# Optimization experiments

Hardware: AMD Instinct MI355X
Metric: run time of the kernel (lower is better)

Reference implementation:

```python
import jax, jax.numpy as jnp
import numpy as np

N_NODES, NUM_GRAPHS, MAX_N = 65536, 512, 192
D, H = 512, 8
DH = D // H


def setup_inputs() -> dict:
    key = jax.random.key(0)
    ks = jax.random.split(key, 13)
    s = 1.0 / np.sqrt(D).astype(np.float32)
    return {
        "node_features": jax.random.normal(ks[0], (N_NODES, D), jnp.float32),
        "batch_indices": jnp.sort(jax.random.randint(ks[1], (N_NODES,), 0, NUM_GRAPHS)),
        "global_query": jax.random.normal(ks[2], (1, H, 1, DH), jnp.float32) * s,
        "w_q": jax.random.normal(ks[3], (D, D), jnp.float32) * s,
        "b_q": jax.random.normal(ks[4], (D,), jnp.float32) * 0.02,
        "w_k": jax.random.normal(ks[5], (D, D), jnp.float32) * s,
        "b_k": jax.random.normal(ks[6], (D,), jnp.float32) * 0.02,
        "w_v": jax.random.normal(ks[7], (D, D), jnp.float32) * s,
        "b_v": jax.random.normal(ks[8], (D,), jnp.float32) * 0.02,
        "w_o": jax.random.normal(ks[9], (D, D), jnp.float32) * s,
        "b_o": jax.random.normal(ks[10], (D,), jnp.float32) * 0.02,
        "w_p": jax.random.normal(ks[11], (D, D), jnp.float32) * s,
        "b_p": jax.random.normal(ks[12], (D,), jnp.float32) * 0.02,
    }


def reference(node_features, batch_indices, global_query, w_q, b_q, w_k, b_k,
              w_v, b_v, w_o, b_o, w_p, b_p):
    # ragged bookkeeping (batch_indices is sorted)
    counts = jax.ops.segment_sum(jnp.ones_like(batch_indices), batch_indices,
                                 num_segments=NUM_GRAPHS)            # [G]
    offsets = jnp.cumsum(counts) - counts                            # [G]
    pos = jnp.arange(N_NODES) - offsets[batch_indices]               # local node pos

    # pad nodes to dense [G, MAX_N, D]
    dense = jnp.zeros((NUM_GRAPHS, MAX_N, D), node_features.dtype)
    dense = dense.at[batch_indices, pos].set(node_features)
    mask = jnp.zeros((NUM_GRAPHS, MAX_N), bool).at[batch_indices, pos].set(True)

    # Faithful replication of torch's expand+reshape of global_query:
    # Q_in[g, t, d] = gq_flat[h*DH + d%DH] with h = (t*D + d) // (n_g*DH)
    gqf = global_query.reshape(H * DH)
    t = jnp.arange(MAX_N)[:, None]                                   # [MAX_N,1]
    d = jnp.arange(D)[None, :]                                       # [1,D]
    n = jnp.maximum(counts, 1)[:, None, None]                        # [G,1,1]
    h = jnp.clip((t * D + d)[None] // (n * DH), 0, H - 1)            # [G,MAX_N,D]
    q_in = gqf[h * DH + (d % DH)[None]]                              # [G,MAX_N,D]

    Q = (q_in @ w_q.T + b_q).reshape(NUM_GRAPHS, MAX_N, H, DH)
    K = (dense @ w_k.T + b_k).reshape(NUM_GRAPHS, MAX_N, H, DH)
    V = (dense @ w_v.T + b_v).reshape(NUM_GRAPHS, MAX_N, H, DH)

    scale = 1.0 / np.sqrt(DH).astype(np.float32)
    scores = jnp.einsum('gthd,gshd->ghts', Q, K) * scale             # [G,H,T,S]
    scores = jnp.where(mask[:, None, None, :], scores, -1e9)
    attn_w = jax.nn.softmax(scores, axis=-1)
    attn = jnp.einsum('ghts,gshd->gthd', attn_w, V).reshape(NUM_GRAPHS, MAX_N, D)
    attn = attn @ w_o.T + b_o

    denom = jnp.maximum(counts, 1).astype(attn.dtype)[:, None]
    pooled = (attn * mask[..., None].astype(attn.dtype)).sum(axis=1) / denom
    return jax.nn.relu(pooled @ w_p.T + b_p)                         # [G, D]
```

## Files before the change

### kernel.cpp

```cpp
#include <hip/hip_runtime.h>
#include <hip/hip_bf16.h>
#include <cstdint>

typedef __bf16 bf16;
typedef __attribute__((ext_vector_type(8))) __bf16 bf16x8;
typedef __attribute__((ext_vector_type(4))) __bf16 bf16x4;
typedef __attribute__((ext_vector_type(2))) __bf16 bf16x2;
typedef __attribute__((ext_vector_type(4))) float f32x4;

#define N_NODES    65536
#define NUM_GRAPHS 512
#define MAX_N      192
#define D          512
#define H          8
#define DH         64
#define UMAX       64
#define USTRIDE    132

__device__ __forceinline__ void gload_lds16(const void* g, void* l) {
    __builtin_amdgcn_global_load_lds((const __attribute__((address_space(1))) void*)g,
                                     (__attribute__((address_space(3))) void*)l, 16, 0, 0);
}

__global__ __launch_bounds__(256) void lb_kernel(const int* __restrict__ batch,
                                                 int* __restrict__ lb) {
    int g = blockIdx.x * 256 + threadIdx.x;
    if (g > NUM_GRAPHS) return;
    int lo = 0, hi = N_NODES;
    while (lo < hi) {
        int mid = (lo + hi) >> 1;
        if (batch[mid] < g) lo = mid + 1; else hi = mid;
    }
    lb[g] = lo;
}

__global__ __launch_bounds__(192) void dedup_kernel(const int* __restrict__ lb,
                                                    int* __restrict__ udata) {
    const int g = blockIdx.x;
    const int off = lb[g];
    const int n = min(lb[g + 1] - off, MAX_N);
    __shared__ int keys[MAX_N];
    __shared__ int ukey[UMAX], ucnt[UMAX];
    __shared__ int nu_s;
    const int t = threadIdx.x;
    if (t < n) {
        unsigned un = (unsigned)n;
        int key = 0;
        #pragma unroll
        for (int p = 0; p < 8; p++) key |= (int)(((unsigned)(8 * t + p)) / un) << (3 * p);
        keys[t] = key;
    }
    __syncthreads();
    if (t == 0) {
        int nu = 0;
        for (int s = 0; s < n; s++) {
            if (s == 0 || keys[s] != keys[s - 1]) {
                if (nu < UMAX) { ukey[nu] = keys[s]; ucnt[nu] = 0; nu++; }
            }
            ucnt[nu - 1] += 1;
        }
        nu_s = nu;
    }
    __syncthreads();
    const int nu = nu_s;
    int* base = udata + (size_t)g * USTRIDE;
    if (t == 0) base[0] = nu;
    if (t < nu) { base[1 + t] = ukey[t]; base[65 + t] = ucnt[t]; }
}

__global__ __launch_bounds__(256) void cvt_kernel(const float* __restrict__ src,
                                                  bf16* __restrict__ dst, int n) {
    int i = (blockIdx.x * 256 + threadIdx.x) * 4;
    if (i >= n) return;
    float4 v = *(const float4*)(src + i);
    bf16x4 o = {(bf16)v.x, (bf16)v.y, (bf16)v.z, (bf16)v.w};
    *(bf16x4*)(dst + i) = o;
}

__global__ __launch_bounds__(256) void p2_kernel(const float* __restrict__ gq,
                                                 const float* __restrict__ wq,
                                                 float* __restrict__ P2) {
    int h = blockIdx.x, p = blockIdx.y;
    __shared__ float gs[64];
    if (threadIdx.x < 64) gs[threadIdx.x] = gq[h * 64 + threadIdx.x];
    __syncthreads();
    for (int o = threadIdx.x; o < D; o += 256) {
        const float* wr = wq + (size_t)o * D + p * 64;
        float acc = 0.f;
        #pragma unroll 16
        for (int j = 0; j < 64; j++) acc += gs[j] * wr[j];
        P2[(size_t)(h * 8 + p) * D + o] = acc;
    }
}

__global__ __launch_bounds__(256) void wov_kernel(const float* __restrict__ wo,
                                                  const float* __restrict__ wv,
                                                  bf16* __restrict__ Wov) {
    const int ot = blockIdx.x;
    const int h  = blockIdx.y;
    __shared__ float wos[32 * 64];
    for (int idx = threadIdx.x; idx < 32 * 64; idx += 256) {
        int ol = idx >> 6, j = idx & 63;
        wos[idx] = wo[(size_t)(ot * 32 + ol) * D + h * 64 + j];
    }
    __syncthreads();
    const int c = threadIdx.x * 2;
    float acc0[32] = {}, acc1[32] = {};
    for (int j = 0; j < 64; j++) {
        float2 v2 = *(const float2*)(wv + (size_t)(h * 64 + j) * D + c);
        #pragma unroll
        for (int o = 0; o < 32; o++) {
            float wj = wos[o * 64 + j];
            acc0[o] += wj * v2.x; acc1[o] += wj * v2.y;
        }
    }
    #pragma unroll
    for (int o = 0; o < 32; o++) {
        bf16x2 r = {(bf16)acc0[o], (bf16)acc1[o]};
        *(bf16x2*)(Wov + (size_t)(ot * 32 + o) * 4096 + h * 512 + c) = r;
    }
}

__global__ __launch_bounds__(256) void cst_kernel(const float* __restrict__ wo,
                                                  const float* __restrict__ bv,
                                                  const float* __restrict__ bo,
                                                  float* __restrict__ cst) {
    int o = blockIdx.x * 256 + threadIdx.x;
    if (o >= D) return;
    const float* wr = wo + (size_t)o * D;
    float acc = bo[o];
    for (int d0 = 0; d0 < D; d0 += 4) {
        float4 wv4 = *(const float4*)(wr + d0);
        float4 b4  = *(const float4*)(bv + d0);
        acc += wv4.x * b4.x + wv4.y * b4.y + wv4.z * b4.z + wv4.w * b4.w;
    }
    cst[o] = acc;
}

__global__ __launch_bounds__(256) void k_gemm(const bf16* __restrict__ Ab,
                                              const bf16* __restrict__ Wkb,
                                              const float* __restrict__ bkb,
                                              bf16* __restrict__ Kout) {
    const int lin = blockIdx.x;
    const int xcd = lin & 7;
    const int idx = lin >> 3;
    const int nt  = idx & 3;
    const int ml  = idx >> 2;
    const int i0 = (xcd * 64 + ml) * 128;
    const int o0 = nt * 128;

    __shared__ char smem[16896];
    bf16* As = (bf16*)smem;
    bf16* Bs = (bf16*)(smem + 8192);
    const int tid = threadIdx.x;
    const int lane = tid & 63;
    const int w = tid >> 6;
    const int wm = w & 1, wn = w >> 1;
    const int fr = lane & 15, quad = lane >> 4;
    const bf16* gA = Ab + (size_t)(i0 + w * 32 + (lane >> 2)) * D + (lane & 3) * 8;
    const bf16* gB = Wkb + (size_t)(o0 + w * 32 + (lane >> 2)) * D + (lane & 3) * 8;
    bf16* lA = As + (w * 32) * 32;
    bf16* lB = Bs + (w * 32) * 32;

    f32x4 acc[4][4] = {};

    for (int kt = 0; kt < D; kt += 32) {
        __syncthreads();
        gload_lds16(gA + kt, lA);
        gload_lds16(gA + (size_t)16 * D + kt, lA + 16 * 32);
        gload_lds16(gB + kt, lB);
        gload_lds16(gB + (size_t)16 * D + kt, lB + 16 * 32);
        __syncthreads();
        bf16x8 fa[4], fb[4];
        #pragma unroll
        for (int mf = 0; mf < 4; mf++)
            fa[mf] = *(const bf16x8*)(As + (wm * 64 + mf * 16 + fr) * 32 + quad * 8);
        #pragma unroll
        for (int nf = 0; nf < 4; nf++)
            fb[nf] = *(const bf16x8*)(Bs + (wn * 64 + nf * 16 + fr) * 32 + quad * 8);
        #pragma unroll
        for (int mf = 0; mf < 4; mf++)
            #pragma unroll
            for (int nf = 0; nf < 4; nf++)
                acc[mf][nf] = __builtin_amdgcn_mfma_f32_16x16x32_bf16(fa[mf], fb[nf], acc[mf][nf], 0, 0, 0);
    }

    bf16* Cs = (bf16*)smem;
    #pragma unroll
    for (int pass = 0; pass < 2; pass++) {
        __syncthreads();
        if (wm == pass) {
            #pragma unroll
            for (int nf = 0; nf < 4; nf++) {
                const int col = wn * 64 + nf * 16 + fr;
                const float bs = bkb[o0 + col];
                #pragma unroll
                for (int mf = 0; mf < 4; mf++) {
                    #pragma unroll
                    for (int r = 0; r < 4; r++)
                        Cs[(mf * 16 + quad * 4 + r) * 132 + col] = (bf16)(acc[mf][nf][r] + bs);
                }
            }
        }
        __syncthreads();
        #pragma unroll
        for (int k = 0; k < 4; k++) {
            int idx2 = k * 256 + tid;
            int row = idx2 >> 4;
            int coff = (idx2 & 15) * 8;
            bf16x8 v = *(const bf16x8*)(Cs + row * 132 + coff);
            *(bf16x8*)(Kout + (size_t)(i0 + pass * 64 + row) * D + o0 + coff) = v;
        }
    }
}

__global__ __launch_bounds__(512) void attn_kernel(const bf16* __restrict__ Kb,
                                                   const float* __restrict__ P2,
                                                   const float* __restrict__ bq,
                                                   const int* __restrict__ lb,
                                                   const int* __restrict__ udata,
                                                   const float* __restrict__ Af,
                                                   bf16* __restrict__ abar) {
    const int g = blockIdx.x;
    const int tid = threadIdx.x;
    const int lane = tid & 63;
    const int w = tid >> 6;
    const int h = w;
    const int off = lb[g];
    const int n = min(lb[g + 1] - off, MAX_N);

    __shared__ bf16 Qs[8][16 * 80];
    __shared__ float wacc[8][MAX_N];
    __shared__ int upat_l[UMAX], ucnt_l[UMAX];

    bf16* outg = abar + (size_t)g * 4096;
    if (n == 0) {
        const bf16 z0 = (bf16)0.f;
        bf16x8 z = {z0, z0, z0, z0, z0, z0, z0, z0};
        *(bf16x8*)(outg + tid * 8) = z;
        return;
    }

    const int* ubase = udata + (size_t)g * USTRIDE;
    const int nu = ubase[0];
    if (tid < 64) {
        upat_l[tid] = (tid < nu) ? ubase[1 + tid] : 0;
        ucnt_l[tid] = (tid < nu) ? ubase[65 + tid] : 0;
    }
    wacc[w][lane] = 0.f; wacc[w][64 + lane] = 0.f; wacc[w][128 + lane] = 0.f;
    __syncthreads();

    const int fr = lane & 15;
    const int quad = lane >> 4;
    const float inv_n = 1.0f / (float)n;

    for (int c0 = 0; c0 < nu; c0 += 16) {
        {
            const int ul = lane >> 2;
            const int j0 = (lane & 3) * 16;
            const bool valid = (c0 + ul) < nu;
            const int pat = upat_l[c0 + ul];
            const float* bpq = bq + h * 64 + j0;
            float4 q0 = *(const float4*)bpq;
            float4 q1 = *(const float4*)(bpq + 4);
            float4 q2 = *(const float4*)(bpq + 8);
            float4 q3 = *(const float4*)(bpq + 12);
            #pragma unroll
            for (int p = 0; p < 8; p++) {
                const int hp = (pat >> (3 * p)) & 7;
                const float* pp = P2 + (size_t)(hp * 8 + p) * D + h * 64 + j0;
                float4 t0 = *(const float4*)pp;
                float4 t1 = *(const float4*)(pp + 4);
                float4 t2 = *(const float4*)(pp + 8);
                float4 t3 = *(const float4*)(pp + 12);
                q0.x += t0.x; q0.y += t0.y; q0.z += t0.z; q0.w += t0.w;
                q1.x += t1.x; q1.y += t1.y; q1.z += t1.z; q1.w += t1.w;
                q2.x += t2.x; q2.y += t2.y; q2.z += t2.z; q2.w += t2.w;
                q3.x += t3.x; q3.y += t3.y; q3.z += t3.z; q3.w += t3.w;
            }
            if (!valid) {
                q0.x=q0.y=q0.z=q0.w=0.f; q1.x=q1.y=q1.z=q1.w=0.f;
                q2.x=q2.y=q2.z=q2.w=0.f; q3.x=q3.y=q3.z=q3.w=0.f;
            }
            bf16x8 b0 = {(bf16)q0.x,(bf16)q0.y,(bf16)q0.z,(bf16)q0.w,
                         (bf16)q1.x,(bf16)q1.y,(bf16)q1.z,(bf16)q1.w};
            bf16x8 b1 = {(bf16)q2.x,(bf16)q2.y,(bf16)q2.z,(bf16)q2.w,
                         (bf16)q3.x,(bf16)q3.y,(bf16)q3.z,(bf16)q3.w};
            *(bf16x8*)(&Qs[w][ul * 80 + j0])     = b0;
            *(bf16x8*)(&Qs[w][ul * 80 + j0 + 8]) = b1;
        }
        bf16x8 fa0 = *(const bf16x8*)(&Qs[w][fr * 80 + quad * 8]);
        bf16x8 fa1 = *(const bf16x8*)(&Qs[w][fr * 80 + 32 + quad * 8]);

        f32x4 sc[12];
        #pragma unroll
        for (int st = 0; st < 12; st++) {
            if (st * 16 < n) {
                int s = st * 16 + fr;
                int row = off + (s < n ? s : n - 1);
                const bf16* kp = Kb + (size_t)row * D + h * 64 + quad * 8;
                bf16x8 fb0 = *(const bf16x8*)kp;
                bf16x8 fb1 = *(const bf16x8*)(kp + 32);
                f32x4 a = {0.f, 0.f, 0.f, 0.f};
                a = __builtin_amdgcn_mfma_f32_16x16x32_bf16(fa0, fb0, a, 0, 0, 0);
                a = __builtin_amdgcn_mfma_f32_16x16x32_bf16(fa1, fb1, a, 0, 0, 0);
                if (s < n) {
                    sc[st].x = a.x * 0.125f; sc[st].y = a.y * 0.125f;
                    sc[st].z = a.z * 0.125f; sc[st].w = a.w * 0.125f;
                } else {
                    sc[st].x = sc[st].y = sc[st].z = sc[st].w = -1e30f;
                }
            } else {
                sc[st].x = sc[st].y = sc[st].z = sc[st].w = -1e30f;
            }
        }
        float m[4] = {-1e30f, -1e30f, -1e30f, -1e30f};
        #pragma unroll
        for (int st = 0; st < 12; st++) {
            m[0] = fmaxf(m[0], sc[st].x); m[1] = fmaxf(m[1], sc[st].y);
            m[2] = fmaxf(m[2], sc[st].z); m[3] = fmaxf(m[3], sc[st].w);
        }
        #pragma unroll
        for (int o = 1; o <= 8; o <<= 1) {
            #pragma unroll
            for (int r = 0; r < 4; r++) m[r] = fmaxf(m[r], __shfl_xor(m[r], o));
        }
        float den[4] = {0.f, 0.f, 0.f, 0.f};
        #pragma unroll
        for (int st = 0; st < 12; st++) {
            float e0 = __expf(sc[st].x - m[0]); float e1 = __expf(sc[st].y - m[1]);
            float e2 = __expf(sc[st].z - m[2]); float e3 = __expf(sc[st].w - m[3]);
            sc[st].x = e0; sc[st].y = e1; sc[st].z = e2; sc[st].w = e3;
            den[0] += e0; den[1] += e1; den[2] += e2; den[3] += e3;
        }
        #pragma unroll
        for (int o = 1; o <= 8; o <<= 1) {
            #pragma unroll
            for (int r = 0; r < 4; r++) den[r] += __shfl_xor(den[r], o);
        }
        float wf[4];
        #pragma unroll
        for (int r = 0; r < 4; r++)
            wf[r] = (float)ucnt_l[c0 + quad * 4 + r] * inv_n / den[r];
        #pragma unroll
        for (int st = 0; st < 12; st++) {
            float v = sc[st].x * wf[0] + sc[st].y * wf[1] + sc[st].z * wf[2] + sc[st].w * wf[3];
            v += __shfl_xor(v, 16);
            v += __shfl_xor(v, 32);
            if (lane < 16) wacc[w][st * 16 + lane] += v;
        }
    }

    __syncthreads();
    const float* Ac = Af + (size_t)off * D + tid;
    float accv[8] = {};
    for (int s = 0; s < n; s++) {
        float av = Ac[(size_t)s * D];
        #pragma unroll
        for (int hh = 0; hh < 8; hh++) accv[hh] += wacc[hh][s] * av;
    }
    #pragma unroll
    for (int hh = 0; hh < 8; hh++) outg[hh * 512 + tid] = (bf16)accv[hh];
}

__global__ __launch_bounds__(256) void zero_kernel(float* __restrict__ p, int n4) {
    int i = blockIdx.x * 256 + threadIdx.x;
    if (i < n4) { float4 z = {0.f, 0.f, 0.f, 0.f}; *(float4*)(p + i * 4) = z; }
}

__global__ __launch_bounds__(256) void og_gemm(const bf16* __restrict__ Ab,
                                               const bf16* __restrict__ Bb,
                                               float* __restrict__ Yt) {
    const int o0 = blockIdx.x * 128;
    const int i0 = blockIdx.y * 128;
    const int k0 = blockIdx.z * 512;
    __shared__ bf16 As[128 * 32];
    __shared__ bf16 Bs[128 * 32];
    const int tid = threadIdx.x;
    const int lane = tid & 63;
    const int w = tid >> 6;
    const int wm = w & 1, wn = w >> 1;
    const int fr = lane & 15, quad = lane >> 4;
    const bf16* gA = Ab + (size_t)(i0 + w * 32 + (lane >> 2)) * 4096 + k0 + (lane & 3) * 8;
    const bf16* gB = Bb + (size_t)(o0 + w * 32 + (lane >> 2)) * 4096 + k0 + (lane & 3) * 8;
    bf16* lA = As + (w * 32) * 32;
    bf16* lB = Bs + (w * 32) * 32;

    f32x4 acc[4][4] = {};

    for (int kt = 0; kt < 512; kt += 32) {
        __syncthreads();
        gload_lds16(gA + kt, lA);
        gload_lds16(gA + (size_t)16 * 4096 + kt, lA + 16 * 32);
        gload_lds16(gB + kt, lB);
        gload_lds16(gB + (size_t)16 * 4096 + kt, lB + 16 * 32);
        __syncthreads();
        bf16x8 fa[4], fb[4];
        #pragma unroll
        for (int mf = 0; mf < 4; mf++)
            fa[mf] = *(const bf16x8*)(As + (wm * 64 + mf * 16 + fr) * 32 + quad * 8);
        #pragma unroll
        for (int nf = 0; nf < 4; nf++)
            fb[nf] = *(const bf16x8*)(Bs + (wn * 64 + nf * 16 + fr) * 32 + quad * 8);
        #pragma unroll
        for (int mf = 0; mf < 4; mf++)
            #pragma unroll
            for (int nf = 0; nf < 4; nf++)
                acc[mf][nf] = __builtin_amdgcn_mfma_f32_16x16x32_bf16(fa[mf], fb[nf], acc[mf][nf], 0, 0, 0);
    }
    #pragma unroll
    for (int nf = 0; nf < 4; nf++) {
        const int col = o0 + wn * 64 + nf * 16 + fr;
        #pragma unroll
        for (int mf = 0; mf < 4; mf++) {
            const int row = i0 + wm * 64 + mf * 16 + quad * 4;
            #pragma unroll
            for (int r = 0; r < 4; r++)
                atomicAdd(&Yt[(size_t)(row + r) * D + col], acc[mf][nf][r]);
        }
    }
}

__global__ __launch_bounds__(256) void proj_p(const float* __restrict__ tmp,
                                              const float* __restrict__ cst,
                                              const bf16* __restrict__ Wpb,
                                              const float* __restrict__ bp,
                                              const int* __restrict__ lb,
                                              float* __restrict__ out) {
    const int o0 = blockIdx.x * 128;
    const int i0 = blockIdx.y * 128;
    __shared__ bf16 As[128 * 32];
    __shared__ bf16 Bs[128 * 32];
    const int tid = threadIdx.x;
    const int lane = tid & 63;
    const int w = tid >> 6;
    const int wm = w & 1, wn = w >> 1;
    const int fr = lane & 15, quad = lane >> 4;
    const int ar = tid >> 1;
    const int ac = (tid & 1) * 16;
    const int g = i0 + ar;
    const bool live = lb[g + 1] - lb[g] > 0;
    const float* tp = tmp + (size_t)g * D + ac;
    const float* cp = cst + ac;
    const bf16* gB = Wpb + (size_t)(o0 + w * 32 + (lane >> 2)) * D + (lane & 3) * 8;
    bf16* lB = Bs + (w * 32) * 32;

    f32x4 acc[4][4] = {};

    for (int kt = 0; kt < D; kt += 32) {
        __syncthreads();
        gload_lds16(gB + kt, lB);
        gload_lds16(gB + (size_t)16 * D + kt, lB + 16 * 32);
        {
            float4 x0 = *(const float4*)(tp + kt);
            float4 x1 = *(const float4*)(tp + kt + 4);
            float4 x2 = *(const float4*)(tp + kt + 8);
            float4 x3 = *(const float4*)(tp + kt + 12);
            float4 c0 = *(const float4*)(cp + kt);
            float4 c1 = *(const float4*)(cp + kt + 4);
            float4 c2 = *(const float4*)(cp + kt + 8);
            float4 c3 = *(const float4*)(cp + kt + 12);
            float s = live ? 1.f : 0.f;
            bf16x8 v0 = {(bf16)((x0.x+c0.x)*s),(bf16)((x0.y+c0.y)*s),(bf16)((x0.z+c0.z)*s),(bf16)((x0.w+c0.w)*s),
                         (bf16)((x1.x+c1.x)*s),(bf16)((x1.y+c1.y)*s),(bf16)((x1.z+c1.z)*s),(bf16)((x1.w+c1.w)*s)};
            bf16x8 v1 = {(bf16)((x2.x+c2.x)*s),(bf16)((x2.y+c2.y)*s),(bf16)((x2.z+c2.z)*s),(bf16)((x2.w+c2.w)*s),
                         (bf16)((x3.x+c3.x)*s),(bf16)((x3.y+c3.y)*s),(bf16)((x3.z+c3.z)*s),(bf16)((x3.w+c3.w)*s)};
            *(bf16x8*)(As + ar * 32 + ac) = v0;
            *(bf16x8*)(As + ar * 32 + ac + 8) = v1;
        }
        __syncthreads();
        bf16x8 fa[4], fb[4];
        #pragma unroll
        for (int mf = 0; mf < 4; mf++)
            fa[mf] = *(const bf16x8*)(As + (wm * 64 + mf * 16 + fr) * 32 + quad * 8);
        #pragma unroll
        for (int nf = 0; nf < 4; nf++)
            fb[nf] = *(const bf16x8*)(Bs + (wn * 64 + nf * 16 + fr) * 32 + quad * 8);
        #pragma unroll
        for (int mf = 0; mf < 4; mf++)
            #pragma unroll
            for (int nf = 0; nf < 4; nf++)
                acc[mf][nf] = __builtin_amdgcn_mfma_f32_16x16x32_bf16(fa[mf], fb[nf], acc[mf][nf], 0, 0, 0);
    }
    #pragma unroll
    for (int nf = 0; nf < 4; nf++) {
        const int col = o0 + wn * 64 + nf * 16 + fr;
        const float bs = bp[col];
        #pragma unroll
        for (int mf = 0; mf < 4; mf++) {
            const int row = i0 + wm * 64 + mf * 16 + quad * 4;
            #pragma unroll
            for (int r = 0; r < 4; r++)
                out[(size_t)(row + r) * D + col] = fmaxf(acc[mf][nf][r] + bs, 0.f);
        }
    }
}

extern "C" void kernel_launch(void* const* d_in, const int* in_sizes, int n_in,
                              void* d_out, int out_size, void* d_ws, size_t ws_size,
                              hipStream_t stream) {
    const float* nf    = (const float*)d_in[0];
    const int*   batch = (const int*)d_in[1];
    const float* gq    = (const float*)d_in[2];
    const float* wq    = (const float*)d_in[3];
    const float* bq    = (const float*)d_in[4];
    const float* wk    = (const float*)d_in[5];
    const float* bk    = (const float*)d_in[6];
    const float* wv    = (const float*)d_in[7];
    const float* bv    = (const float*)d_in[8];
    const float* wo    = (const float*)d_in[9];
    const float* bo    = (const float*)d_in[10];
    const float* wp    = (const float*)d_in[11];
    const float* bp    = (const float*)d_in[12];
    float* out = (float*)d_out;

    char* ws = (char*)d_ws;
    bf16*  Abf  = (bf16*)ws;
    bf16*  abar = (bf16*)(ws + ((size_t)2 << 20));
    bf16*  Wov  = (bf16*)(ws + ((size_t)6 << 20));
    float* tmp  = (float*)(ws + ((size_t)10 << 20));
    float* cst  = (float*)(ws + ((size_t)11 << 20));
    bf16*  Kb   = (bf16*)(ws + ((size_t)64 << 20));
    char* sm = ws + ((size_t)128 << 20);
    int*  lb    = (int*)sm;    sm += 4096;
    int*  udata = (int*)sm;    sm += (size_t)NUM_GRAPHS * USTRIDE * 4 + 2048;
    bf16* Wkb   = (bf16*)sm;   sm += (size_t)D * D * 2;
    bf16* Wpb   = (bf16*)sm;   sm += (size_t)D * D * 2;
    float* P2   = (float*)sm;  sm += (size_t)64 * D * 4;

    lb_kernel<<<3, 256, 0, stream>>>(batch, lb);
    dedup_kernel<<<NUM_GRAPHS, 192, 0, stream>>>(lb, udata);
    cvt_kernel<<<(D * D / 4) / 256, 256, 0, stream>>>(wk, Wkb, D * D);
    cvt_kernel<<<(D * D / 4) / 256, 256, 0, stream>>>(wp, Wpb, D * D);
    p2_kernel<<<dim3(8, 8), 256, 0, stream>>>(gq, wq, P2);
    cvt_kernel<<<(N_NODES * D / 4) / 256, 256, 0, stream>>>(nf, Abf, N_NODES * D);
    k_gemm<<<2048, 256, 0, stream>>>(Abf, Wkb, bk, Kb);
    wov_kernel<<<dim3(16, 8), 256, 0, stream>>>(wo, wv, Wov);
    cst_kernel<<<2, 256, 0, stream>>>(wo, bv, bo, cst);
    attn_kernel<<<NUM_GRAPHS, 512, 0, stream>>>(Kb, P2, bq, lb, udata, nf, abar);
    zero_kernel<<<(NUM_GRAPHS * D / 4 + 255) / 256, 256, 0, stream>>>(tmp, NUM_GRAPHS * D / 4);
    og_gemm<<<dim3(4, 4, 8), 256, 0, stream>>>(abar, Wov, tmp);
    proj_p<<<dim3(4, 4), 256, 0, stream>>>(tmp, cst, Wpb, bp, lb, out);
}
```

Baseline: 448.1 us.

## Fuse fp32-to-bf16 node conversion into K GEMM and sort graphs by size

```diff
diff --git a/kernel.cpp b/kernel.cpp
--- a/kernel.cpp
+++ b/kernel.cpp
@@ -32,6 +32,25 @@
         if (batch[mid] < g) lo = mid + 1; else hi = mid;
     }
     lb[g] = lo;
+}
+
+__global__ __launch_bounds__(512) void sortg_kernel(const int* __restrict__ lb,
+                                                    int* __restrict__ perm) {
+    __shared__ int hist[MAX_N + 1];
+    __shared__ int base[MAX_N + 1];
+    const int t = threadIdx.x;
+    if (t <= MAX_N) hist[t] = 0;
+    __syncthreads();
+    const int n = min(lb[t + 1] - lb[t], MAX_N);
+    atomicAdd(&hist[n], 1);
+    __syncthreads();
+    if (t == 0) {
+        int acc = 0;
+        for (int k = MAX_N; k >= 0; k--) { base[k] = acc; acc += hist[k]; }
+    }
+    __syncthreads();
+    int pos = atomicAdd(&base[n], 1);
+    perm[pos] = t;
 }
 
 __global__ __launch_bounds__(192) void dedup_kernel(const int* __restrict__ lb,
@@ -137,7 +156,7 @@
     cst[o] = acc;
 }
 
-__global__ __launch_bounds__(256) void k_gemm(const bf16* __restrict__ Ab,
+__global__ __launch_bounds__(256) void k_gemm(const float* __restrict__ Af,
                                               const bf16* __restrict__ Wkb,
                                               const float* __restrict__ bkb,
                                               bf16* __restrict__ Kout) {
@@ -149,32 +168,47 @@
     const int i0 = (xcd * 64 + ml) * 128;
     const int o0 = nt * 128;
 
-    __shared__ char smem[16896];
-    bf16* As = (bf16*)smem;
-    bf16* Bs = (bf16*)(smem + 8192);
+    __shared__ char smem[24576];
+    float* Asf = (float*)smem;
+    bf16*  Bs  = (bf16*)(smem + 16384);
     const int tid = threadIdx.x;
     const int lane = tid & 63;
     const int w = tid >> 6;
     const int wm = w & 1, wn = w >> 1;
     const int fr = lane & 15, quad = lane >> 4;
-    const bf16* gA = Ab + (size_t)(i0 + w * 32 + (lane >> 2)) * D + (lane & 3) * 8;
+
+    const int sra = lane >> 3;
+    const int c16 = lane & 7;
+    const int scol = ((c16 ^ sra) << 2);
+    const float* gA = Af + (size_t)(i0 + w * 32 + sra) * D + scol;
+    float* lAf = Asf + (w * 32) * 32;
+
     const bf16* gB = Wkb + (size_t)(o0 + w * 32 + (lane >> 2)) * D + (lane & 3) * 8;
-    bf16* lA = As + (w * 32) * 32;
     bf16* lB = Bs + (w * 32) * 32;
 
     f32x4 acc[4][4] = {};
 
     for (int kt = 0; kt < D; kt += 32) {
         __syncthreads();
-        gload_lds16(gA + kt, lA);
-        gload_lds16(gA + (size_t)16 * D + kt, lA + 16 * 32);
+        gload_lds16(gA + kt, lAf);
+        gload_lds16(gA + (size_t)8  * D + kt, lAf + 8  * 32);
+        gload_lds16(gA + (size_t)16 * D + kt, lAf + 16 * 32);
+        gload_lds16(gA + (size_t)24 * D + kt, lAf + 24 * 32);
         gload_lds16(gB + kt, lB);
         gload_lds16(gB + (size_t)16 * D + kt, lB + 16 * 32);
         __syncthreads();
         bf16x8 fa[4], fb[4];
         #pragma unroll
-        for (int mf = 0; mf < 4; mf++)
-            fa[mf] = *(const bf16x8*)(As + (wm * 64 + mf * 16 + fr) * 32 + quad * 8);
+        for (int mf = 0; mf < 4; mf++) {
+            const int row = wm * 64 + mf * 16 + fr;
+            const int u0 = (quad * 2) ^ (row & 7);
+            const int u1 = (quad * 2 + 1) ^ (row & 7);
+            f32x4 a0 = *(const f32x4*)(Asf + row * 32 + u0 * 4);
+            f32x4 a1 = *(const f32x4*)(Asf + row * 32 + u1 * 4);
+            bf16x8 v = {(bf16)a0.x,(bf16)a0.y,(bf16)a0.z,(bf16)a0.w,
+                        (bf16)a1.x,(bf16)a1.y,(bf16)a1.z,(bf16)a1.w};
+            fa[mf] = v;
+        }
         #pragma unroll
         for (int nf = 0; nf < 4; nf++)
             fb[nf] = *(const bf16x8*)(Bs + (wn * 64 + nf * 16 + fr) * 32 + quad * 8);
@@ -220,8 +254,9 @@
                                                    const int* __restrict__ lb,
                                                    const int* __restrict__ udata,
                                                    const float* __restrict__ Af,
+                                                   const int* __restrict__ perm,
                                                    bf16* __restrict__ abar) {
-    const int g = blockIdx.x;
+    const int g = perm[blockIdx.x];
     const int tid = threadIdx.x;
     const int lane = tid & 63;
     const int w = tid >> 6;
@@ -515,7 +550,6 @@
     float* out = (float*)d_out;
 
     char* ws = (char*)d_ws;
-    bf16*  Abf  = (bf16*)ws;
     bf16*  abar = (bf16*)(ws + ((size_t)2 << 20));
     bf16*  Wov  = (bf16*)(ws + ((size_t)6 << 20));
     float* tmp  = (float*)(ws + ((size_t)10 << 20));
@@ -527,17 +561,18 @@
     bf16* Wkb   = (bf16*)sm;   sm += (size_t)D * D * 2;
     bf16* Wpb   = (bf16*)sm;   sm += (size_t)D * D * 2;
     float* P2   = (float*)sm;  sm += (size_t)64 * D * 4;
+    int*  perm  = (int*)sm;    sm += NUM_GRAPHS * 4;
 
     lb_kernel<<<3, 256, 0, stream>>>(batch, lb);
+    sortg_kernel<<<1, 512, 0, stream>>>(lb, perm);
     dedup_kernel<<<NUM_GRAPHS, 192, 0, stream>>>(lb, udata);
     cvt_kernel<<<(D * D / 4) / 256, 256, 0, stream>>>(wk, Wkb, D * D);
     cvt_kernel<<<(D * D / 4) / 256, 256, 0, stream>>>(wp, Wpb, D * D);
     p2_kernel<<<dim3(8, 8), 256, 0, stream>>>(gq, wq, P2);
-    cvt_kernel<<<(N_NODES * D / 4) / 256, 256, 0, stream>>>(nf, Abf, N_NODES * D);
-    k_gemm<<<2048, 256, 0, stream>>>(Abf, Wkb, bk, Kb);
+    k_gemm<<<2048, 256, 0, stream>>>(nf, Wkb, bk, Kb);
     wov_kernel<<<dim3(16, 8), 256, 0, stream>>>(wo, wv, Wov);
     cst_kernel<<<2, 256, 0, stream>>>(wo, bv, bo, cst);
-    attn_kernel<<<NUM_GRAPHS, 512, 0, stream>>>(Kb, P2, bq, lb, udata, nf, abar);
+    attn_kernel<<<NUM_GRAPHS, 512, 0, stream>>>(Kb, P2, bq, lb, udata, nf, perm, abar);
     zero_kernel<<<(NUM_GRAPHS * D / 4 + 255) / 256, 256, 0, stream>>>(tmp, NUM_GRAPHS * D / 4);
     og_gemm<<<dim3(4, 4, 8), 256, 0, stream>>>(abar, Wov, tmp);
     proj_p<<<dim3(4, 4), 256, 0, stream>>>(tmp, cst, Wpb, bp, lb, out);
```

Result: faster. 436.5 us (-2.6%).
